# Kernel tuning notes

Hardware: AMD Instinct MI355X
Metric: run time of the kernel (lower is better)

## Reference

```python
import jax, jax.numpy as jnp
import numpy as np

ALPHA = 20.0 / 100.0  # dt / tau
NOISE_SCALE = 0.1 * (2.0 * ALPHA) ** 0.5  # network_noise * sqrt(2*alpha)

T, B, I, H, O = 512, 64, 128, 512, 64


def setup_inputs() -> dict:
    key = jax.random.key(0)
    ks = jax.random.split(key, 6)
    s_in = 1.0 / np.sqrt(I)
    s_h = 1.0 / np.sqrt(H)
    return {
        "x": jax.random.normal(ks[0], (T, B, I), jnp.float32),
        "noise": jax.random.normal(ks[1], (T, B, H), jnp.float32),
        "W_in": jax.random.normal(ks[2], (H, I), jnp.float32) * s_in,
        "W_rec": jax.random.normal(ks[3], (H, H), jnp.float32) * s_h,
        "b_rec": jnp.zeros((H,), jnp.float32),
        "W_out": jax.random.normal(ks[4], (O, H), jnp.float32) * s_h,
        "b_out": jnp.zeros((O,), jnp.float32),
    }


def reference(x, noise, W_in, W_rec, b_rec, W_out, b_out):
    # Precompute input projection for all timesteps: (T, B, H)
    xin = jnp.einsum("tbi,hi->tbh", x, W_in)

    def step(hidden, inp):
        xin_t, noise_t = inp
        h_new = jax.nn.relu(xin_t + hidden @ W_rec.T + b_rec)
        h_new = hidden * (1.0 - ALPHA) + h_new * ALPHA
        h_new = h_new + noise_t * NOISE_SCALE
        return h_new, h_new

    h0 = jnp.zeros((x.shape[1], W_rec.shape[0]), x.dtype)
    _, rnn_output = jax.lax.scan(step, h0, (xin, noise))  # (T, B, H)
    output = jnp.einsum("tbh,oh->tbo", rnn_output, W_out) + b_out
    return output, rnn_output
```

## Files before the change

### kernel.cpp

```cpp
#include <hip/hip_runtime.h>

constexpr int T  = 512;
constexpr int NB = 64;
constexpr int NI = 128;
constexpr int NH = 512;
constexpr int NO = 64;

constexpr float ALPHA = 0.2f;
constexpr float NSC   = 0.063245553203367586f;

typedef _Float16 h2_t __attribute__((ext_vector_type(2)));

#if defined(__has_builtin)
#  if __has_builtin(__builtin_amdgcn_fdot2)
#    define HAS_FDOT2 1
#  endif
#endif
#ifndef HAS_FDOT2
#  define HAS_FDOT2 0
#endif

__device__ __forceinline__ float dot2(uint32_t wbits, uint32_t hbits, float acc) {
#if HAS_FDOT2
    return __builtin_amdgcn_fdot2(__builtin_bit_cast(h2_t, wbits),
                                  __builtin_bit_cast(h2_t, hbits), acc, false);
#else
    const h2_t wv = __builtin_bit_cast(h2_t, wbits);
    const h2_t hv = __builtin_bit_cast(h2_t, hbits);
    return acc + (float)wv.x * (float)hv.x + (float)wv.y * (float)hv.y;
#endif
}

__device__ __forceinline__ uint32_t pk2(float x, float y) {
    return __builtin_bit_cast(uint32_t, (h2_t){(_Float16)x, (_Float16)y});
}

__global__ __launch_bounds__(256) void k_gemm_nt_bias(
    const float* __restrict__ A, const float* __restrict__ Bm,
    const float* __restrict__ bias, float* __restrict__ C,
    int M, int N, int K)
{
    __shared__ __align__(16) float As[32][68];
    __shared__ __align__(16) float Bs[32][68];
    const int tid = threadIdx.x;
    const int tx = tid & 15, ty = tid >> 4;
    const long row0 = (long)blockIdx.x * 64;
    const long col0 = (long)blockIdx.y * 64;
    const int lr = tid >> 3;
    const int lq = tid & 7;

    float acc[4][4] = {};

    for (int kt = 0; kt < K; kt += 32) {
        #pragma unroll
        for (int hh = 0; hh < 2; ++hh) {
            const int r = lr + hh * 32;
            const float4 va = *(const float4*)&A[(size_t)(row0 + r) * K + kt + lq * 4];
            As[lq*4+0][r] = va.x; As[lq*4+1][r] = va.y;
            As[lq*4+2][r] = va.z; As[lq*4+3][r] = va.w;
            const float4 vb = *(const float4*)&Bm[(size_t)(col0 + r) * K + kt + lq * 4];
            Bs[lq*4+0][r] = vb.x; Bs[lq*4+1][r] = vb.y;
            Bs[lq*4+2][r] = vb.z; Bs[lq*4+3][r] = vb.w;
        }
        __syncthreads();
        #pragma unroll
        for (int kk = 0; kk < 32; ++kk) {
            const float4 a4 = *(const float4*)&As[kk][ty * 4];
            const float4 b4 = *(const float4*)&Bs[kk][tx * 4];
            const float a[4] = {a4.x, a4.y, a4.z, a4.w};
            const float b[4] = {b4.x, b4.y, b4.z, b4.w};
            #pragma unroll
            for (int i = 0; i < 4; ++i)
                #pragma unroll
                for (int j = 0; j < 4; ++j)
                    acc[i][j] += a[i] * b[j];
        }
        __syncthreads();
    }

    #pragma unroll
    for (int i = 0; i < 4; ++i) {
        const long r = row0 + ty * 4 + i;
        const int  cc = (int)col0 + tx * 4;
        float4 ov;
        ov.x = acc[i][0] + bias[cc + 0];
        ov.y = acc[i][1] + bias[cc + 1];
        ov.z = acc[i][2] + bias[cc + 2];
        ov.w = acc[i][3] + bias[cc + 3];
        *(float4*)&C[(size_t)r * N + cc] = ov;
    }
}

__device__ __forceinline__ uint32_t pack_h(float h, uint32_t tag) {
    const _Float16 hf = (_Float16)h;
    const uint32_t hb = __builtin_bit_cast(unsigned short, hf);
    return (hb << 16) | (tag & 0xFFFFu);
}

__global__
__attribute__((amdgpu_flat_work_group_size(512, 512)))
__attribute__((amdgpu_waves_per_eu(2, 2)))
void k_rnn(
    const float* __restrict__ W_rec,
    const float* __restrict__ noise,
    float* __restrict__ rnn,
    uint32_t* __restrict__ ex)
{
    const int bid = blockIdx.x;
    const int g = bid & 63;
    const int m = bid >> 6;
    const int tid = threadIdx.x;
    const int w = tid >> 6;
    const int l = tid & 63;

    __shared__ __align__(16) unsigned short hbf[NH];
    __shared__ __align__(16) float pr[8][128];

    uint32_t wa0,wa1,wa2,wa3,wa4,wa5,wa6,wa7,wa8,wa9,wa10,wa11,wa12,wa13,wa14,wa15,
             wa16,wa17,wa18,wa19,wa20,wa21,wa22,wa23,wa24,wa25,wa26,wa27,wa28,wa29,wa30,wa31;
    uint32_t wb0,wb1,wb2,wb3,wb4,wb5,wb6,wb7,wb8,wb9,wb10,wb11,wb12,wb13,wb14,wb15,
             wb16,wb17,wb18,wb19,wb20,wb21,wb22,wb23,wb24,wb25,wb26,wb27,wb28,wb29,wb30,wb31;
    {
        const float* p0 = W_rec + (size_t)(m * 128 + l) * NH + w * 64;
        const float* p1 = W_rec + (size_t)(m * 128 + l + 64) * NH + w * 64;
#define LDW(P, VA, VB, OFF) { const float4 q_ = *(const float4*)((P) + (OFF)); \
                              VA = pk2(q_.x, q_.y); VB = pk2(q_.z, q_.w); }
        LDW(p0, wa0,  wa1,   0) LDW(p0, wa2,  wa3,   4)
        LDW(p0, wa4,  wa5,   8) LDW(p0, wa6,  wa7,  12)
        LDW(p0, wa8,  wa9,  16) LDW(p0, wa10, wa11, 20)
        LDW(p0, wa12, wa13, 24) LDW(p0, wa14, wa15, 28)
        LDW(p0, wa16, wa17, 32) LDW(p0, wa18, wa19, 36)
        LDW(p0, wa20, wa21, 40) LDW(p0, wa22, wa23, 44)
        LDW(p0, wa24, wa25, 48) LDW(p0, wa26, wa27, 52)
        LDW(p0, wa28, wa29, 56) LDW(p0, wa30, wa31, 60)
        LDW(p1, wb0,  wb1,   0) LDW(p1, wb2,  wb3,   4)
        LDW(p1, wb4,  wb5,   8) LDW(p1, wb6,  wb7,  12)
        LDW(p1, wb8,  wb9,  16) LDW(p1, wb10, wb11, 20)
        LDW(p1, wb12, wb13, 24) LDW(p1, wb14, wb15, 28)
        LDW(p1, wb16, wb17, 32) LDW(p1, wb18, wb19, 36)
        LDW(p1, wb20, wb21, 40) LDW(p1, wb22, wb23, 44)
        LDW(p1, wb24, wb25, 48) LDW(p1, wb26, wb27, 52)
        LDW(p1, wb28, wb29, 56) LDW(p1, wb30, wb31, 60)
#undef LDW
    }
#define PIN8(A,B,C,D,E,F,G,H) asm volatile("" : "+v"(A),"+v"(B),"+v"(C),"+v"(D),"+v"(E),"+v"(F),"+v"(G),"+v"(H));
    PIN8(wa0,wa1,wa2,wa3,wa4,wa5,wa6,wa7)
    PIN8(wa8,wa9,wa10,wa11,wa12,wa13,wa14,wa15)
    PIN8(wa16,wa17,wa18,wa19,wa20,wa21,wa22,wa23)
    PIN8(wa24,wa25,wa26,wa27,wa28,wa29,wa30,wa31)
    PIN8(wb0,wb1,wb2,wb3,wb4,wb5,wb6,wb7)
    PIN8(wb8,wb9,wb10,wb11,wb12,wb13,wb14,wb15)
    PIN8(wb16,wb17,wb18,wb19,wb20,wb21,wb22,wb23)
    PIN8(wb24,wb25,wb26,wb27,wb28,wb29,wb30,wb31)
#undef PIN8

    const int gc = m * 128 + tid;

    const int q    = tid - 128;
    const int pp   = q >> 7;
    const int pm   = pp + (pp >= m ? 1 : 0);
    const int pcol = pm * 128 + (q & 127);

    hbf[tid] = 0;

    float hreg = 0.f;

    float xin_pf = 0.f, noi_pf = 0.f;
    if (tid < 128) {
        xin_pf = rnn[(size_t)g * NH + gc];
        noi_pf = noise[(size_t)g * NH + gc];
    }
    __syncthreads();

    int alive  = 1;
    int budget = 1 << 16;

    for (int t = 0; t < T; ++t) {
        float aA0 = 0.f, aA1 = 0.f, aB0 = 0.f, aB1 = 0.f;
        {
            const uint4* hp = (const uint4*)&hbf[w * 64];
#define DOTB(N, A0, A1, A2, A3) { const uint4 u_ = hp[N]; \
            aA0 = dot2(wa##A0, u_.x, aA0); aA1 = dot2(wa##A1, u_.y, aA1); \
            aA0 = dot2(wa##A2, u_.z, aA0); aA1 = dot2(wa##A3, u_.w, aA1); \
            aB0 = dot2(wb##A0, u_.x, aB0); aB1 = dot2(wb##A1, u_.y, aB1); \
            aB0 = dot2(wb##A2, u_.z, aB0); aB1 = dot2(wb##A3, u_.w, aB1); }
            DOTB(0,  0,  1,  2,  3)
            DOTB(1,  4,  5,  6,  7)
            DOTB(2,  8,  9, 10, 11)
            DOTB(3, 12, 13, 14, 15)
            DOTB(4, 16, 17, 18, 19)
            DOTB(5, 20, 21, 22, 23)
            DOTB(6, 24, 25, 26, 27)
            DOTB(7, 28, 29, 30, 31)
#undef DOTB
        }
        pr[w][l]      = aA0 + aA1;
        pr[w][l + 64] = aB0 + aB1;
        __syncthreads();

        const uint32_t want = (uint32_t)(t + 1);
        uint32_t* slot = ex + (size_t)(t & 1) * NB * NH;

        if (tid < 128) {
            float sum = 0.f;
            #pragma unroll
            for (int k = 0; k < 8; ++k) sum += pr[k][tid];
            const float hn = fmaxf(xin_pf + sum, 0.f);
            const float nw = (1.f - ALPHA) * hreg + ALPHA * hn + NSC * noi_pf;
            hreg = nw;
            const uint32_t pk = pack_h(nw, want);
            (void)__hip_atomic_exchange(&slot[(size_t)g * NH + gc], pk,
                                        __ATOMIC_RELAXED, __HIP_MEMORY_SCOPE_AGENT);
            hbf[gc] = (unsigned short)(pk >> 16);
            rnn[((size_t)t * NB + g) * NH + gc] = nw;
            const int tn = (t + 1 < T) ? (t + 1) : t;
            xin_pf = rnn[((size_t)tn * NB + g) * NH + gc];
            noi_pf = noise[((size_t)tn * NB + g) * NH + gc];
        } else {
            uint32_t v;
            if (alive) {
                for (;;) {
                    v = __hip_atomic_fetch_or(&slot[(size_t)g * NH + pcol], 0u,
                                              __ATOMIC_RELAXED, __HIP_MEMORY_SCOPE_AGENT);
                    if ((v & 0xFFFFu) == (want & 0xFFFFu)) break;
                    __builtin_amdgcn_s_sleep(1);
                    if (--budget < 0) { alive = 0; break; }
                }
            } else {
                v = __hip_atomic_fetch_or(&slot[(size_t)g * NH + pcol], 0u,
                                          __ATOMIC_RELAXED, __HIP_MEMORY_SCOPE_AGENT);
            }
            hbf[pcol] = (unsigned short)(v >> 16);
        }
        __syncthreads();
    }
}

extern "C" void kernel_launch(void* const* d_in, const int* in_sizes, int n_in,
                              void* d_out, int out_size, void* d_ws, size_t ws_size,
                              hipStream_t stream)
{
    (void)in_sizes; (void)n_in; (void)out_size; (void)ws_size;
    const float* x     = (const float*)d_in[0];
    const float* noise = (const float*)d_in[1];
    const float* W_in  = (const float*)d_in[2];
    const float* W_rec = (const float*)d_in[3];
    const float* b_rec = (const float*)d_in[4];
    const float* W_out = (const float*)d_in[5];
    const float* b_out = (const float*)d_in[6];

    float* out = (float*)d_out;
    float* rnn = out + (size_t)T * NB * NO;

    uint32_t* ex = (uint32_t*)d_ws;

    hipMemsetAsync(ex, 0, (size_t)2 * NB * NH * sizeof(uint32_t), stream);

    hipLaunchKernelGGL(k_gemm_nt_bias, dim3((T * NB) / 64, NH / 64), dim3(256), 0, stream,
                       x, W_in, b_rec, rnn, T * NB, NH, NI);

    hipLaunchKernelGGL(k_rnn, dim3(256), dim3(512), 0, stream,
                       W_rec, noise, rnn, ex);

    hipLaunchKernelGGL(k_gemm_nt_bias, dim3((T * NB) / 64, NO / 64), dim3(256), 0, stream,
                       rnn, W_out, b_out, out, T * NB, NO, NH);
}
```

Measured before the change: 718.2 us.

## Stream recurrent weights from LDS and pre-packed global buffer instead of registers

Moves the recurrent weight slice out of the 64 pinned VGPRs per thread. Part of it now lives in shared memory and the rest in a pre-packed fp16 global buffer, which a new prep kernel builds and the loop re-reads every timestep. The aim is to free registers, for occupancy or scheduling, by dropping the waves_per_eu constraint. The cost is extra LDS traffic and L2/global loads on the latency-critical recurrent step, plus one extra launch. The old register-resident kernel stays as a fallback when the workspace is too small.

```diff
diff --git a/kernel.cpp b/kernel.cpp
--- a/kernel.cpp
+++ b/kernel.cpp
@@ -97,15 +97,38 @@
     return (hb << 16) | (tag & 0xFFFFu);
 }
 
-__global__
-__attribute__((amdgpu_flat_work_group_size(512, 512)))
-__attribute__((amdgpu_waves_per_eu(2, 2)))
-void k_rnn(
+__global__ __launch_bounds__(256) void k_prep(
+    const float* __restrict__ W_rec, uint4* __restrict__ wq)
+{
+    const int idx = blockIdx.x * 256 + threadIdx.x;
+    const int l  = idx & 63;
+    const int t5 = idx >> 6;
+    const int jj = t5 % 10;
+    const int u  = t5 / 10;
+    const int w  = u & 7;
+    const int m  = u >> 3;
+    const int col = m * 128 + l + (jj >= 5 ? 64 : 0);
+    const int p0  = 12 + 4 * (jj % 5);
+    const float* src = W_rec + (size_t)col * NH + w * 64 + 2 * p0;
+    const float4 a = *(const float4*)(src);
+    const float4 b = *(const float4*)(src + 4);
+    uint4 o;
+    o.x = pk2(a.x, a.y); o.y = pk2(a.z, a.w);
+    o.z = pk2(b.x, b.y); o.w = pk2(b.z, b.w);
+    wq[idx] = o;
+}
+
+__global__ __launch_bounds__(512) void k_rnn_dual(
     const float* __restrict__ W_rec,
     const float* __restrict__ noise,
     float* __restrict__ rnn,
-    uint32_t* __restrict__ ex)
+    uint32_t* __restrict__ ex,
+    const uint4* __restrict__ wq)
 {
+    __shared__ __align__(16) uint4 WL[8][6][64];
+    __shared__ __align__(16) unsigned short hbf[NH];
+    __shared__ __align__(16) float pr[8][128];
+
     const int bid = blockIdx.x;
     const int g = bid & 63;
     const int m = bid >> 6;
@@ -113,46 +136,25 @@
     const int w = tid >> 6;
     const int l = tid & 63;
 
-    __shared__ __align__(16) unsigned short hbf[NH];
-    __shared__ __align__(16) float pr[8][128];
-
-    uint32_t wa0,wa1,wa2,wa3,wa4,wa5,wa6,wa7,wa8,wa9,wa10,wa11,wa12,wa13,wa14,wa15,
-             wa16,wa17,wa18,wa19,wa20,wa21,wa22,wa23,wa24,wa25,wa26,wa27,wa28,wa29,wa30,wa31;
-    uint32_t wb0,wb1,wb2,wb3,wb4,wb5,wb6,wb7,wb8,wb9,wb10,wb11,wb12,wb13,wb14,wb15,
-             wb16,wb17,wb18,wb19,wb20,wb21,wb22,wb23,wb24,wb25,wb26,wb27,wb28,wb29,wb30,wb31;
     {
         const float* p0 = W_rec + (size_t)(m * 128 + l) * NH + w * 64;
         const float* p1 = W_rec + (size_t)(m * 128 + l + 64) * NH + w * 64;
-#define LDW(P, VA, VB, OFF) { const float4 q_ = *(const float4*)((P) + (OFF)); \
-                              VA = pk2(q_.x, q_.y); VB = pk2(q_.z, q_.w); }
-        LDW(p0, wa0,  wa1,   0) LDW(p0, wa2,  wa3,   4)
-        LDW(p0, wa4,  wa5,   8) LDW(p0, wa6,  wa7,  12)
-        LDW(p0, wa8,  wa9,  16) LDW(p0, wa10, wa11, 20)
-        LDW(p0, wa12, wa13, 24) LDW(p0, wa14, wa15, 28)
-        LDW(p0, wa16, wa17, 32) LDW(p0, wa18, wa19, 36)
-        LDW(p0, wa20, wa21, 40) LDW(p0, wa22, wa23, 44)
-        LDW(p0, wa24, wa25, 48) LDW(p0, wa26, wa27, 52)
-        LDW(p0, wa28, wa29, 56) LDW(p0, wa30, wa31, 60)
-        LDW(p1, wb0,  wb1,   0) LDW(p1, wb2,  wb3,   4)
-        LDW(p1, wb4,  wb5,   8) LDW(p1, wb6,  wb7,  12)
-        LDW(p1, wb8,  wb9,  16) LDW(p1, wb10, wb11, 20)
-        LDW(p1, wb12, wb13, 24) LDW(p1, wb14, wb15, 28)
-        LDW(p1, wb16, wb17, 32) LDW(p1, wb18, wb19, 36)
-        LDW(p1, wb20, wb21, 40) LDW(p1, wb22, wb23, 44)
-        LDW(p1, wb24, wb25, 48) LDW(p1, wb26, wb27, 52)
-        LDW(p1, wb28, wb29, 56) LDW(p1, wb30, wb31, 60)
-#undef LDW
-    }
-#define PIN8(A,B,C,D,E,F,G,H) asm volatile("" : "+v"(A),"+v"(B),"+v"(C),"+v"(D),"+v"(E),"+v"(F),"+v"(G),"+v"(H));
-    PIN8(wa0,wa1,wa2,wa3,wa4,wa5,wa6,wa7)
-    PIN8(wa8,wa9,wa10,wa11,wa12,wa13,wa14,wa15)
-    PIN8(wa16,wa17,wa18,wa19,wa20,wa21,wa22,wa23)
-    PIN8(wa24,wa25,wa26,wa27,wa28,wa29,wa30,wa31)
-    PIN8(wb0,wb1,wb2,wb3,wb4,wb5,wb6,wb7)
-    PIN8(wb8,wb9,wb10,wb11,wb12,wb13,wb14,wb15)
-    PIN8(wb16,wb17,wb18,wb19,wb20,wb21,wb22,wb23)
-    PIN8(wb24,wb25,wb26,wb27,wb28,wb29,wb30,wb31)
-#undef PIN8
+        #pragma unroll
+        for (int jj = 0; jj < 3; ++jj) {
+            const float4 qa = *(const float4*)(p0 + jj * 8);
+            const float4 qb = *(const float4*)(p0 + jj * 8 + 4);
+            uint4 ca;
+            ca.x = pk2(qa.x, qa.y); ca.y = pk2(qa.z, qa.w);
+            ca.z = pk2(qb.x, qb.y); ca.w = pk2(qb.z, qb.w);
+            WL[w][jj][l] = ca;
+            const float4 qc = *(const float4*)(p1 + jj * 8);
+            const float4 qd = *(const float4*)(p1 + jj * 8 + 4);
+            uint4 cb;
+            cb.x = pk2(qc.x, qc.y); cb.y = pk2(qc.z, qc.w);
+            cb.z = pk2(qd.x, qd.y); cb.w = pk2(qd.z, qd.w);
+            WL[w][3 + jj][l] = cb;
+        }
+    }
 
     const int gc = m * 128 + tid;
 
@@ -161,6 +163,8 @@
     const int pm   = pp + (pp >= m ? 1 : 0);
     const int pcol = pm * 128 + (q & 127);
 
+    const uint4* wbase = wq + (size_t)(m * 8 + w) * 10 * 64;
+
     hbf[tid] = 0;
 
     float hreg = 0.f;
@@ -175,25 +179,39 @@
     int alive  = 1;
     int budget = 1 << 16;
 
+#define DOT4(W4, H4, A0, A1) \
+    A0 = dot2((W4).x, (H4).x, A0); A1 = dot2((W4).y, (H4).y, A1); \
+    A0 = dot2((W4).z, (H4).z, A0); A1 = dot2((W4).w, (H4).w, A1);
+
     for (int t = 0; t < T; ++t) {
+        int off = l;
+        asm volatile("" : "+v"(off));
+
+        const uint4 v0 = wbase[0 * 64 + off];
+        const uint4 v1 = wbase[1 * 64 + off];
+        const uint4 v2 = wbase[2 * 64 + off];
+        const uint4 v3 = wbase[3 * 64 + off];
+        const uint4 v4 = wbase[4 * 64 + off];
+        const uint4 v5 = wbase[5 * 64 + off];
+        const uint4 v6 = wbase[6 * 64 + off];
+        const uint4 v7 = wbase[7 * 64 + off];
+        const uint4 v8 = wbase[8 * 64 + off];
+        const uint4 v9 = wbase[9 * 64 + off];
+
+        const uint4* hp = (const uint4*)&hbf[w * 64];
+        const uint4 h0 = hp[0], h1 = hp[1], h2 = hp[2], h3 = hp[3];
+        const uint4 h4 = hp[4], h5 = hp[5], h6 = hp[6], h7 = hp[7];
+        const uint4 A0 = WL[w][0][off], A1 = WL[w][1][off], A2 = WL[w][2][off];
+        const uint4 B0 = WL[w][3][off], B1 = WL[w][4][off], B2 = WL[w][5][off];
+
         float aA0 = 0.f, aA1 = 0.f, aB0 = 0.f, aB1 = 0.f;
-        {
-            const uint4* hp = (const uint4*)&hbf[w * 64];
-#define DOTB(N, A0, A1, A2, A3) { const uint4 u_ = hp[N]; \
-            aA0 = dot2(wa##A0, u_.x, aA0); aA1 = dot2(wa##A1, u_.y, aA1); \
-            aA0 = dot2(wa##A2, u_.z, aA0); aA1 = dot2(wa##A3, u_.w, aA1); \
-            aB0 = dot2(wb##A0, u_.x, aB0); aB1 = dot2(wb##A1, u_.y, aB1); \
-            aB0 = dot2(wb##A2, u_.z, aB0); aB1 = dot2(wb##A3, u_.w, aB1); }
-            DOTB(0,  0,  1,  2,  3)
-            DOTB(1,  4,  5,  6,  7)
-            DOTB(2,  8,  9, 10, 11)
-            DOTB(3, 12, 13, 14, 15)
-            DOTB(4, 16, 17, 18, 19)
-            DOTB(5, 20, 21, 22, 23)
-            DOTB(6, 24, 25, 26, 27)
-            DOTB(7, 28, 29, 30, 31)
-#undef DOTB
-        }
+        DOT4(A0, h0, aA0, aA1) DOT4(A1, h1, aA0, aA1) DOT4(A2, h2, aA0, aA1)
+        DOT4(B0, h0, aB0, aB1) DOT4(B1, h1, aB0, aB1) DOT4(B2, h2, aB0, aB1)
+        DOT4(v0, h3, aA0, aA1) DOT4(v1, h4, aA0, aA1) DOT4(v2, h5, aA0, aA1)
+        DOT4(v3, h6, aA0, aA1) DOT4(v4, h7, aA0, aA1)
+        DOT4(v5, h3, aB0, aB1) DOT4(v6, h4, aB0, aB1) DOT4(v7, h5, aB0, aB1)
+        DOT4(v8, h6, aB0, aB1) DOT4(v9, h7, aB0, aB1)
+
         pr[w][l]      = aA0 + aA1;
         pr[w][l + 64] = aB0 + aB1;
         __syncthreads();
@@ -234,13 +252,138 @@
         }
         __syncthreads();
     }
+#undef DOT4
+}
+
+__global__
+__attribute__((amdgpu_flat_work_group_size(512, 512)))
+__attribute__((amdgpu_waves_per_eu(2, 2)))
+void k_rnn_fb(
+    const float* __restrict__ W_rec, const float* __restrict__ noise,
+    float* __restrict__ rnn, uint32_t* __restrict__ ex)
+{
+    const int bid = blockIdx.x;
+    const int g = bid & 63;
+    const int m = bid >> 6;
+    const int tid = threadIdx.x;
+    const int w = tid >> 6;
+    const int l = tid & 63;
+
+    __shared__ __align__(16) unsigned short hbf[NH];
+    __shared__ __align__(16) float pr[8][128];
+
+    uint32_t wa0,wa1,wa2,wa3,wa4,wa5,wa6,wa7,wa8,wa9,wa10,wa11,wa12,wa13,wa14,wa15,
+             wa16,wa17,wa18,wa19,wa20,wa21,wa22,wa23,wa24,wa25,wa26,wa27,wa28,wa29,wa30,wa31;
+    uint32_t wb0,wb1,wb2,wb3,wb4,wb5,wb6,wb7,wb8,wb9,wb10,wb11,wb12,wb13,wb14,wb15,
+             wb16,wb17,wb18,wb19,wb20,wb21,wb22,wb23,wb24,wb25,wb26,wb27,wb28,wb29,wb30,wb31;
+    {
+        const float* p0 = W_rec + (size_t)(m * 128 + l) * NH + w * 64;
+        const float* p1 = W_rec + (size_t)(m * 128 + l + 64) * NH + w * 64;
+#define LDW(P, VA, VB, OFF) { const float4 q_ = *(const float4*)((P) + (OFF)); \
+                              VA = pk2(q_.x, q_.y); VB = pk2(q_.z, q_.w); }
+        LDW(p0, wa0,  wa1,   0) LDW(p0, wa2,  wa3,   4)
+        LDW(p0, wa4,  wa5,   8) LDW(p0, wa6,  wa7,  12)
+        LDW(p0, wa8,  wa9,  16) LDW(p0, wa10, wa11, 20)
+        LDW(p0, wa12, wa13, 24) LDW(p0, wa14, wa15, 28)
+        LDW(p0, wa16, wa17, 32) LDW(p0, wa18, wa19, 36)
+        LDW(p0, wa20, wa21, 40) LDW(p0, wa22, wa23, 44)
+        LDW(p0, wa24, wa25, 48) LDW(p0, wa26, wa27, 52)
+        LDW(p0, wa28, wa29, 56) LDW(p0, wa30, wa31, 60)
+        LDW(p1, wb0,  wb1,   0) LDW(p1, wb2,  wb3,   4)
+        LDW(p1, wb4,  wb5,   8) LDW(p1, wb6,  wb7,  12)
+        LDW(p1, wb8,  wb9,  16) LDW(p1, wb10, wb11, 20)
+        LDW(p1, wb12, wb13, 24) LDW(p1, wb14, wb15, 28)
+        LDW(p1, wb16, wb17, 32) LDW(p1, wb18, wb19, 36)
+        LDW(p1, wb20, wb21, 40) LDW(p1, wb22, wb23, 44)
+        LDW(p1, wb24, wb25, 48) LDW(p1, wb26, wb27, 52)
+        LDW(p1, wb28, wb29, 56) LDW(p1, wb30, wb31, 60)
+#undef LDW
+    }
+
+    const int gc = m * 128 + tid;
+    const int q    = tid - 128;
+    const int pp   = q >> 7;
+    const int pm   = pp + (pp >= m ? 1 : 0);
+    const int pcol = pm * 128 + (q & 127);
+
+    hbf[tid] = 0;
+    float hreg = 0.f;
+    float xin_pf = 0.f, noi_pf = 0.f;
+    if (tid < 128) {
+        xin_pf = rnn[(size_t)g * NH + gc];
+        noi_pf = noise[(size_t)g * NH + gc];
+    }
+    __syncthreads();
+
+    int alive  = 1;
+    int budget = 1 << 16;
+
+    for (int t = 0; t < T; ++t) {
+        float aA0 = 0.f, aA1 = 0.f, aB0 = 0.f, aB1 = 0.f;
+        {
+            const uint4* hp = (const uint4*)&hbf[w * 64];
+#define DOTB(N, A0, A1, A2, A3) { const uint4 u_ = hp[N]; \
+            aA0 = dot2(wa##A0, u_.x, aA0); aA1 = dot2(wa##A1, u_.y, aA1); \
+            aA0 = dot2(wa##A2, u_.z, aA0); aA1 = dot2(wa##A3, u_.w, aA1); \
+            aB0 = dot2(wb##A0, u_.x, aB0); aB1 = dot2(wb##A1, u_.y, aB1); \
+            aB0 = dot2(wb##A2, u_.z, aB0); aB1 = dot2(wb##A3, u_.w, aB1); }
+            DOTB(0,  0,  1,  2,  3)
+            DOTB(1,  4,  5,  6,  7)
+            DOTB(2,  8,  9, 10, 11)
+            DOTB(3, 12, 13, 14, 15)
+            DOTB(4, 16, 17, 18, 19)
+            DOTB(5, 20, 21, 22, 23)
+            DOTB(6, 24, 25, 26, 27)
+            DOTB(7, 28, 29, 30, 31)
+#undef DOTB
+        }
+        pr[w][l]      = aA0 + aA1;
+        pr[w][l + 64] = aB0 + aB1;
+        __syncthreads();
+
+        const uint32_t want = (uint32_t)(t + 1);
+        uint32_t* slot = ex + (size_t)(t & 1) * NB * NH;
+
+        if (tid < 128) {
+            float sum = 0.f;
+            #pragma unroll
+            for (int k = 0; k < 8; ++k) sum += pr[k][tid];
+            const float hn = fmaxf(xin_pf + sum, 0.f);
+            const float nw = (1.f - ALPHA) * hreg + ALPHA * hn + NSC * noi_pf;
+            hreg = nw;
+            const uint32_t pk = pack_h(nw, want);
+            (void)__hip_atomic_exchange(&slot[(size_t)g * NH + gc], pk,
+                                        __ATOMIC_RELAXED, __HIP_MEMORY_SCOPE_AGENT);
+            hbf[gc] = (unsigned short)(pk >> 16);
+            rnn[((size_t)t * NB + g) * NH + gc] = nw;
+            const int tn = (t + 1 < T) ? (t + 1) : t;
+            xin_pf = rnn[((size_t)tn * NB + g) * NH + gc];
+            noi_pf = noise[((size_t)tn * NB + g) * NH + gc];
+        } else {
+            uint32_t v;
+            if (alive) {
+                for (;;) {
+                    v = __hip_atomic_fetch_or(&slot[(size_t)g * NH + pcol], 0u,
+                                              __ATOMIC_RELAXED, __HIP_MEMORY_SCOPE_AGENT);
+                    if ((v & 0xFFFFu) == (want & 0xFFFFu)) break;
+                    __builtin_amdgcn_s_sleep(1);
+                    if (--budget < 0) { alive = 0; break; }
+                }
+            } else {
+                v = __hip_atomic_fetch_or(&slot[(size_t)g * NH + pcol], 0u,
+                                          __ATOMIC_RELAXED, __HIP_MEMORY_SCOPE_AGENT);
+            }
+            hbf[pcol] = (unsigned short)(v >> 16);
+        }
+        __syncthreads();
+    }
 }
 
 extern "C" void kernel_launch(void* const* d_in, const int* in_sizes, int n_in,
                               void* d_out, int out_size, void* d_ws, size_t ws_size,
                               hipStream_t stream)
 {
-    (void)in_sizes; (void)n_in; (void)out_size; (void)ws_size;
+    (void)in_sizes; (void)n_in; (void)out_size;
     const float* x     = (const float*)d_in[0];
     const float* noise = (const float*)d_in[1];
     const float* W_in  = (const float*)d_in[2];
@@ -253,14 +396,22 @@
     float* rnn = out + (size_t)T * NB * NO;
 
     uint32_t* ex = (uint32_t*)d_ws;
+    uint4*    wq = (uint4*)((char*)d_ws + 262144);
+    const size_t need = 262144 + (size_t)20480 * 16;
 
     hipMemsetAsync(ex, 0, (size_t)2 * NB * NH * sizeof(uint32_t), stream);
 
     hipLaunchKernelGGL(k_gemm_nt_bias, dim3((T * NB) / 64, NH / 64), dim3(256), 0, stream,
                        x, W_in, b_rec, rnn, T * NB, NH, NI);
 
-    hipLaunchKernelGGL(k_rnn, dim3(256), dim3(512), 0, stream,
-                       W_rec, noise, rnn, ex);
+    if (ws_size >= need) {
+        hipLaunchKernelGGL(k_prep, dim3(80), dim3(256), 0, stream, W_rec, wq);
+        hipLaunchKernelGGL(k_rnn_dual, dim3(256), dim3(512), 0, stream,
+                           W_rec, noise, rnn, ex, wq);
+    } else {
+        hipLaunchKernelGGL(k_rnn_fb, dim3(256), dim3(512), 0, stream,
+                           W_rec, noise, rnn, ex);
+    }
 
     hipLaunchKernelGGL(k_gemm_nt_bias, dim3((T * NB) / 64, NO / 64), dim3(256), 0, stream,
                        rnn, W_out, b_out, out, T * NB, NO, NH);
```

Result: slower. 880.3 us (+22.6%).
